# Kernel tuning notes

Hardware: AMD Instinct MI355X
Metric: run time of the kernel (lower is better)

Reference implementation:

```python
import jax, jax.numpy as jnp
import numpy as np

L, C, H, DH, LAT, N, B = 6, 768, 12, 64, 256, 65, 512


def setup_inputs() -> dict:
    key = jax.random.key(0)
    ks = jax.random.split(key, 16)
    def p(k, shape, std=0.02):
        return jax.random.normal(k, shape, jnp.float32) * std
    return {
        "x": jax.random.normal(ks[0], (B, N, C), jnp.float32),
        "ln1_g": jnp.ones((L, C), jnp.float32), "ln1_b": jnp.zeros((L, C), jnp.float32),
        "qkv_w": p(ks[1], (L, C, 3 * C)),
        "proj_w": p(ks[2], (L, C, C)),
        "qn_g": jnp.ones((L, DH), jnp.float32), "qn_b": jnp.zeros((L, DH), jnp.float32),
        "kn_g": jnp.ones((L, DH), jnp.float32), "kn_b": jnp.zeros((L, DH), jnp.float32),
        "sg_w1": p(ks[3], (L, C, 2 * LAT)),
        "sg_ln1_g": jnp.ones((L, 2 * LAT), jnp.float32), "sg_ln1_b": jnp.zeros((L, 2 * LAT), jnp.float32),
        "sg_w2": p(ks[4], (L, 2 * LAT, LAT * H)),
        "sg_ln2_g": jnp.ones((L, LAT * H), jnp.float32), "sg_ln2_b": jnp.zeros((L, LAT * H), jnp.float32),
        "sg_bias_w": p(ks[5], (L, LAT, 65 * 65), std=0.005),
        "ln2_g": jnp.ones((L, C), jnp.float32), "ln2_b": jnp.zeros((L, C), jnp.float32),
        "gate_w": p(ks[6], (L, C, 4 * C)),
        "value_w": p(ks[7], (L, C, 4 * C)),
        "out_w": p(ks[8], (L, 4 * C, C)),
    }


def _ln(x, g, b, eps=1e-5):
    # torch nn.LayerNorm: biased variance
    m = jnp.mean(x, axis=-1, keepdims=True)
    v = jnp.var(x, axis=-1, keepdims=True)
    return (x - m) * jax.lax.rsqrt(v + eps) * g + b


def _block(x, p):
    (l1g, l1b, qkvw, projw, qng, qnb, kng, knb,
     w1, s1g, s1b, w2, s2g, s2b, bw, l2g, l2b, gw, vw, ow) = p
    Bb, Nn, Cc = x.shape
    scale = DH ** -0.5
    h = _ln(x, l1g, l1b)
    cls = h[:, 0]                                     # (B, C)
    qkv = (h @ qkvw).reshape(Bb, Nn, 3, H, DH).transpose(2, 0, 3, 1, 4)
    q, k, v = qkv[0], qkv[1], qkv[2]                  # each (B, H, N, DH)
    q = _ln(q, qng, qnb) * scale
    k = _ln(k, kng, knb)
    attn = jnp.einsum('bhnd,bhmd->bhnm', q, k)        # (B, H, N, N)
    # SmolGen: CLS -> per-head additive bias
    lat1 = jax.nn.silu(_ln(cls @ w1, s1g, s1b))       # (B, 2*LAT)
    lat2 = _ln(lat1 @ w2, s2g, s2b).reshape(Bb, H, LAT)
    bias = (lat2 @ bw).reshape(Bb, H, 65, 65)
    attn = jax.nn.softmax(attn + bias[:, :, :Nn, :Nn], axis=-1)
    o = jnp.einsum('bhnm,bhmd->bhnd', attn, v)
    o = o.transpose(0, 2, 1, 3).reshape(Bb, Nn, Cc)
    x = x + o @ projw
    h2 = _ln(x, l2g, l2b)
    x = x + ((h2 @ gw) * jax.nn.silu(h2 @ vw)) @ ow   # SwiGLU
    return x, None


def reference(x, ln1_g, ln1_b, qkv_w, proj_w, qn_g, qn_b, kn_g, kn_b,
              sg_w1, sg_ln1_g, sg_ln1_b, sg_w2, sg_ln2_g, sg_ln2_b, sg_bias_w,
              ln2_g, ln2_b, gate_w, value_w, out_w):
    params = (ln1_g, ln1_b, qkv_w, proj_w, qn_g, qn_b, kn_g, kn_b,
              sg_w1, sg_ln1_g, sg_ln1_b, sg_w2, sg_ln2_g, sg_ln2_b, sg_bias_w,
              ln2_g, ln2_b, gate_w, value_w, out_w)
    out, _ = jax.lax.scan(_block, x, params)
    return out
```

## Files before the change

### kernel.cpp

```cpp
#include <hip/hip_runtime.h>
#include <hip/hip_bf16.h>


typedef __bf16 v8bf  __attribute__((ext_vector_type(8)));
typedef float  v16f  __attribute__((ext_vector_type(16)));

#define EPI_BF16      0
#define EPI_ADDF32    1
#define EPI_SILU      2
#define EPI_MUL       3
#define EPI_BF16MASK  4

__device__ __forceinline__ v16f mfma32(v8bf a, v8bf b, v16f c) {
  return __builtin_amdgcn_mfma_f32_32x32x16_bf16(a, b, c, 0, 0, 0);
}

template<int EPI>
__global__ __launch_bounds__(256, 3)
void gemm_bt(const __bf16* __restrict__ A, long long lda,
             const __bf16* __restrict__ Bt,
             void* outp, const __bf16* extra,
             int Nout, int K, int nvalid)
{
  __shared__ __align__(16) __bf16 Als[128 * 64];
  __shared__ __align__(16) __bf16 Bls[128 * 64];
  const int tid  = threadIdx.x;
  const int w    = tid >> 6, lane = tid & 63;
  const int m0   = blockIdx.y * 128, n0 = blockIdx.x * 128;
  const int wm   = (w & 1) * 64, wn = (w >> 1) * 64;
  const int l31  = lane & 31, l5 = lane >> 5;

  const __bf16* ag[4];
  const __bf16* bg[4];
#pragma unroll
  for (int i = 0; i < 4; ++i) {
    int li  = i * 256 + tid;
    int row = li >> 3;
    int c   = (li & 7) ^ (row & 7);
    ag[i] = A  + (size_t)(m0 + row) * (size_t)lda + c * 8;
    bg[i] = Bt + (size_t)(n0 + row) * (size_t)K   + c * 8;
  }
  char* alds0 = ((char*)Als) + w * 1024;
  char* blds0 = ((char*)Bls) + w * 1024;

  v16f acc[2][2] = {};

  for (int kt = 0; kt < K; kt += 64) {
#pragma unroll
    for (int i = 0; i < 4; ++i) {
      __builtin_amdgcn_global_load_lds(
          (const __attribute__((address_space(1))) void*)(ag[i]),
          (__attribute__((address_space(3))) void*)(alds0 + i * 4096), 16, 0, 0);
      __builtin_amdgcn_global_load_lds(
          (const __attribute__((address_space(1))) void*)(bg[i]),
          (__attribute__((address_space(3))) void*)(blds0 + i * 4096), 16, 0, 0);
      ag[i] += 64; bg[i] += 64;
    }
    __syncthreads();
#pragma unroll
    for (int kk = 0; kk < 4; ++kk) {
      v8bf af[2], bf[2];
#pragma unroll
      for (int t = 0; t < 2; ++t) {
        int m  = wm + t * 32 + l31;
        int ch = (kk * 2 + l5) ^ (m & 7);
        af[t] = *(const v8bf*)(Als + m * 64 + ch * 8);
        int n   = wn + t * 32 + l31;
        int ch2 = (kk * 2 + l5) ^ (n & 7);
        bf[t] = *(const v8bf*)(Bls + n * 64 + ch2 * 8);
      }
      acc[0][0] = mfma32(af[0], bf[0], acc[0][0]);
      acc[0][1] = mfma32(af[0], bf[1], acc[0][1]);
      acc[1][0] = mfma32(af[1], bf[0], acc[1][0]);
      acc[1][1] = mfma32(af[1], bf[1], acc[1][1]);
    }
    __syncthreads();
  }

#pragma unroll
  for (int mi = 0; mi < 2; ++mi)
#pragma unroll
  for (int ni = 0; ni < 2; ++ni) {
    int col  = n0 + wn + ni * 32 + l31;
    int rowb = m0 + wm + mi * 32 + 4 * l5;
#pragma unroll
    for (int r = 0; r < 16; ++r) {
      int row   = rowb + (r & 3) + 8 * (r >> 2);
      float val = acc[mi][ni][r];
      size_t idx = (size_t)row * (size_t)Nout + col;
      if (EPI == EPI_BF16) {
        ((__bf16*)outp)[idx] = (__bf16)val;
      } else if (EPI == EPI_ADDF32) {
        ((float*)outp)[idx] += val;
      } else if (EPI == EPI_SILU) {
        float s = val / (1.f + __expf(-val));
        ((__bf16*)outp)[idx] = (__bf16)s;
      } else if (EPI == EPI_MUL) {
        float e = (float)extra[idx];
        ((__bf16*)outp)[idx] = (__bf16)(val * e);
      } else {
        if (col < nvalid)
          ((__bf16*)outp)[(size_t)row * (size_t)nvalid + col] = (__bf16)val;
      }
    }
  }
}

__global__ void transpose_w(const float* __restrict__ src, __bf16* __restrict__ dst,
                            int K, int N, int Npad)
{
  __shared__ float t[32][33];
  int n0 = blockIdx.x * 32, k0 = blockIdx.y * 32;
  int tx = threadIdx.x, ty = threadIdx.y;
#pragma unroll
  for (int i = 0; i < 32; i += 8) {
    int k = k0 + ty + i, n = n0 + tx;
    t[ty + i][tx] = (k < K && n < N) ? src[(size_t)k * N + n] : 0.f;
  }
  __syncthreads();
#pragma unroll
  for (int i = 0; i < 32; i += 8) {
    int n = n0 + ty + i, k = k0 + tx;
    if (n < Npad && k < K) dst[(size_t)n * K + k] = (__bf16)t[tx][ty + i];
  }
}

__global__ __launch_bounds__(256)
void ln_f32_to_bf16(const float* __restrict__ x, const float* __restrict__ g,
                    const float* __restrict__ bb, __bf16* __restrict__ out, int C)
{
  __shared__ float sm[8];
  const float* xr = x + (size_t)blockIdx.x * C;
  float sum = 0.f, sq = 0.f;
  for (int i = threadIdx.x; i < C; i += 256) { float v = xr[i]; sum += v; sq += v * v; }
#pragma unroll
  for (int d = 1; d < 64; d <<= 1) { sum += __shfl_xor(sum, d); sq += __shfl_xor(sq, d); }
  if ((threadIdx.x & 63) == 0) { sm[threadIdx.x >> 6] = sum; sm[4 + (threadIdx.x >> 6)] = sq; }
  __syncthreads();
  sum = sm[0] + sm[1] + sm[2] + sm[3];
  sq  = sm[4] + sm[5] + sm[6] + sm[7];
  float mean = sum / C;
  float var  = sq / C - mean * mean;
  float rs   = rsqrtf(var + 1e-5f);
  __bf16* orow = out + (size_t)blockIdx.x * C;
  for (int i = threadIdx.x; i < C; i += 256)
    orow[i] = (__bf16)((xr[i] - mean) * rs * g[i] + bb[i]);
}

__global__ __launch_bounds__(256)
void ln_bf16_kernel(const __bf16* __restrict__ x, const float* __restrict__ g,
                    const float* __restrict__ bb, __bf16* __restrict__ out,
                    int C, int do_silu)
{
  __shared__ float sm[8];
  const __bf16* xr = x + (size_t)blockIdx.x * C;
  float sum = 0.f, sq = 0.f;
  for (int i = threadIdx.x; i < C; i += 256) { float v = (float)xr[i]; sum += v; sq += v * v; }
#pragma unroll
  for (int d = 1; d < 64; d <<= 1) { sum += __shfl_xor(sum, d); sq += __shfl_xor(sq, d); }
  if ((threadIdx.x & 63) == 0) { sm[threadIdx.x >> 6] = sum; sm[4 + (threadIdx.x >> 6)] = sq; }
  __syncthreads();
  sum = sm[0] + sm[1] + sm[2] + sm[3];
  sq  = sm[4] + sm[5] + sm[6] + sm[7];
  float mean = sum / C;
  float var  = sq / C - mean * mean;
  float rs   = rsqrtf(var + 1e-5f);
  __bf16* orow = out + (size_t)blockIdx.x * C;
  for (int i = threadIdx.x; i < C; i += 256) {
    float y = ((float)xr[i] - mean) * rs * g[i] + bb[i];
    if (do_silu) y = y / (1.f + __expf(-y));
    orow[i] = (__bf16)y;
  }
}

__global__ __launch_bounds__(256)
void attn_mfma(const __bf16* __restrict__ qkv,
               const float* __restrict__ qg, const float* __restrict__ qb,
               const float* __restrict__ kg, const float* __restrict__ kb,
               const __bf16* __restrict__ bias, __bf16* __restrict__ o)
{
  __shared__ __align__(16) char smem[58640];
  __bf16* qs = (__bf16*)smem;
  __bf16* ks = (__bf16*)(smem) + 96 * 64;
  __bf16* Ps = (__bf16*)smem;
  __bf16* vt = (__bf16*)(smem + 24576);
  float*  Ss = (float*)(smem + 40960);

  const int tid = threadIdx.x;
  const int bh  = blockIdx.x;
  const int b = bh / 12, h = bh % 12;
  const int w = tid >> 6, lane = tid & 63;
  const int l31 = lane & 31, l5 = lane >> 5;

  const float qgl = qg[lane], qbl = qb[lane];
  const float kgl = kg[lane], kbl = kb[lane];
  for (int n = w; n < 65; n += 4) {
    size_t src = ((size_t)(b * 65 + n)) * 2304 + h * 64 + lane;
    float qv = (float)qkv[src];
    float kv = (float)qkv[src + 768];
    float s1 = qv, s2 = qv * qv, t1 = kv, t2 = kv * kv;
#pragma unroll
    for (int d = 1; d < 64; d <<= 1) {
      s1 += __shfl_xor(s1, d); s2 += __shfl_xor(s2, d);
      t1 += __shfl_xor(t1, d); t2 += __shfl_xor(t2, d);
    }
    float qm = s1 * 0.015625f, qva = s2 * 0.015625f - qm * qm;
    float km = t1 * 0.015625f, kva = t2 * 0.015625f - km * km;
    float qrs = rsqrtf(qva + 1e-5f), krs = rsqrtf(kva + 1e-5f);
    qs[n * 64 + (((lane >> 3) ^ (n & 7)) * 8) + (lane & 7)] =
        (__bf16)(((qv - qm) * qrs * qgl + qbl) * 0.125f);
    ks[n * 64 + (((lane >> 3) ^ (n & 7)) * 8) + (lane & 7)] =
        (__bf16)((kv - km) * krs * kgl + kbl);
    vt[lane * 128 + (((n >> 3) ^ (lane & 7)) * 8) + (n & 7)] = qkv[src + 1536];
  }
  for (int e = tid; e < 64 * 31; e += 256) {
    int d = e / 31, j = 65 + e % 31;
    vt[d * 128 + (((j >> 3) ^ (d & 7)) * 8) + (j & 7)] = (__bf16)0.f;
  }
  __syncthreads();

  const __bf16* bp = bias + (size_t)bh * 4225;
  for (int t = w; t < 9; t += 4) {
    int it = t / 3, jt = t % 3;
    int mrow = it * 32 + l31;
    int nrow = jt * 32 + l31;
    v16f acc = {};
#pragma unroll
    for (int kk = 0; kk < 4; ++kk) {
      v8bf aq = *(const v8bf*)(qs + mrow * 64 + (((kk * 2 + l5) ^ (mrow & 7)) * 8));
      v8bf bk = *(const v8bf*)(ks + nrow * 64 + (((kk * 2 + l5) ^ (nrow & 7)) * 8));
      acc = mfma32(aq, bk, acc);
    }
    int j  = jt * 32 + l31;
    int ib = it * 32 + 4 * l5;
#pragma unroll
    for (int r = 0; r < 16; ++r) {
      int i = ib + (r & 3) + 8 * (r >> 2);
      if (i < 65 && j < 65)
        Ss[i * 68 + j] = acc[r] + (float)bp[i * 65 + j];
    }
  }
  __syncthreads();

  for (int i = w; i < 65; i += 4) {
    float x1 = Ss[i * 68 + lane];
    float x2 = (lane == 0) ? Ss[i * 68 + 64] : -1e30f;
    float mx = fmaxf(x1, x2);
#pragma unroll
    for (int d = 1; d < 64; d <<= 1) mx = fmaxf(mx, __shfl_xor(mx, d));
    float e1 = __expf(x1 - mx);
    float e2 = (lane == 0) ? __expf(x2 - mx) : 0.f;
    float s = e1 + e2;
#pragma unroll
    for (int d = 1; d < 64; d <<= 1) s += __shfl_xor(s, d);
    float inv = 1.f / s;
    Ps[i * 128 + (((lane >> 3) ^ (i & 7)) * 8) + (lane & 7)] = (__bf16)(e1 * inv);
    if (lane < 32) {
      int c2 = 64 + lane;
      float pv2 = (lane == 0) ? e2 * inv : 0.f;
      Ps[i * 128 + (((c2 >> 3) ^ (i & 7)) * 8) + (c2 & 7)] = (__bf16)pv2;
    }
  }
  __syncthreads();

  for (int t = w; t < 6; t += 4) {
    int it = t >> 1, dt = t & 1;
    int prow = it * 32 + l31;
    int drow = dt * 32 + l31;
    v16f acc = {};
#pragma unroll
    for (int kk = 0; kk < 6; ++kk) {
      v8bf ap = *(const v8bf*)(Ps + prow * 128 + (((kk * 2 + l5) ^ (prow & 7)) * 8));
      v8bf bv = *(const v8bf*)(vt + drow * 128 + (((kk * 2 + l5) ^ (drow & 7)) * 8));
      acc = mfma32(ap, bv, acc);
    }
    int d  = dt * 32 + l31;
    int ib = it * 32 + 4 * l5;
#pragma unroll
    for (int r = 0; r < 16; ++r) {
      int i = ib + (r & 3) + 8 * (r >> 2);
      if (i < 65)
        o[((size_t)(b * 65 + i) * 12 + h) * 64 + d] = (__bf16)acc[r];
    }
  }
}

extern "C" void kernel_launch(void* const* d_in, const int* in_sizes, int n_in,
                              void* d_out, int out_size, void* d_ws, size_t ws_size,
                              hipStream_t stream)
{
  (void)in_sizes; (void)n_in; (void)ws_size;
  const float* x_in    = (const float*)d_in[0];
  const float* ln1_g   = (const float*)d_in[1];
  const float* ln1_b   = (const float*)d_in[2];
  const float* qkv_w   = (const float*)d_in[3];
  const float* proj_w  = (const float*)d_in[4];
  const float* qn_g    = (const float*)d_in[5];
  const float* qn_b    = (const float*)d_in[6];
  const float* kn_g    = (const float*)d_in[7];
  const float* kn_b    = (const float*)d_in[8];
  const float* sg_w1   = (const float*)d_in[9];
  const float* sg_ln1g = (const float*)d_in[10];
  const float* sg_ln1b = (const float*)d_in[11];
  const float* sg_w2   = (const float*)d_in[12];
  const float* sg_ln2g = (const float*)d_in[13];
  const float* sg_ln2b = (const float*)d_in[14];
  const float* sg_bw   = (const float*)d_in[15];
  const float* ln2_g   = (const float*)d_in[16];
  const float* ln2_b   = (const float*)d_in[17];
  const float* gate_w  = (const float*)d_in[18];
  const float* value_w = (const float*)d_in[19];
  const float* out_w   = (const float*)d_in[20];

  char* ws = (char*)d_ws;
  size_t off = 0;
  auto alloc = [&](size_t bytes) -> char* {
    char* p = ws + off; off += (bytes + 255) & ~(size_t)255; return p;
  };

  __bf16* wt_qkv  = (__bf16*)alloc(2304ull * 768 * 2);
  __bf16* wt_proj = (__bf16*)alloc(768ull * 768 * 2);
  __bf16* wt_sg1  = (__bf16*)alloc(512ull * 768 * 2);
  __bf16* wt_sg2  = (__bf16*)alloc(3072ull * 512 * 2);
  __bf16* wt_bias = (__bf16*)alloc(4352ull * 256 * 2);
  __bf16* wt_gate = (__bf16*)alloc(3072ull * 768 * 2);
  __bf16* wt_val  = (__bf16*)alloc(3072ull * 768 * 2);
  __bf16* wt_out  = (__bf16*)alloc(768ull * 3072 * 2);
  __bf16* hbuf    = (__bf16*)alloc(33280ull * 768 * 2);
  __bf16* biasbuf = (__bf16*)alloc(6144ull * 4225 * 2);
  __bf16* BIG     = (__bf16*)alloc(33280ull * 2304 * 2);
  __bf16* t1buf   = (__bf16*)alloc(512ull * 512 * 2);
  __bf16* lat1    = (__bf16*)alloc(512ull * 512 * 2);
  __bf16* t2buf   = (__bf16*)alloc(512ull * 3072 * 2);
  __bf16* lat2    = (__bf16*)alloc(512ull * 3072 * 2);

  __bf16* qkvbuf = BIG;
  __bf16* mlpbuf = biasbuf;

  hipMemcpyAsync(d_out, x_in, (size_t)out_size * sizeof(float),
                 hipMemcpyDeviceToDevice, stream);
  float* xb = (float*)d_out;

  dim3 tb(32, 8);
  for (int l = 0; l < 6; ++l) {
    const float* l1g = ln1_g + l * 768;
    const float* l1b = ln1_b + l * 768;
    const float* qg  = qn_g + l * 64;
    const float* qb  = qn_b + l * 64;
    const float* kg  = kn_g + l * 64;
    const float* kb  = kn_b + l * 64;
    const float* s1g = sg_ln1g + l * 512;
    const float* s1b = sg_ln1b + l * 512;
    const float* s2g = sg_ln2g + l * 3072;
    const float* s2b = sg_ln2b + l * 3072;
    const float* l2g = ln2_g + l * 768;
    const float* l2b = ln2_b + l * 768;

    transpose_w<<<dim3(72, 24), tb, 0, stream>>>(qkv_w  + (size_t)l * 768 * 2304, wt_qkv, 768, 2304, 2304);
    transpose_w<<<dim3(24, 24), tb, 0, stream>>>(proj_w + (size_t)l * 768 * 768,  wt_proj, 768, 768, 768);
    transpose_w<<<dim3(16, 24), tb, 0, stream>>>(sg_w1  + (size_t)l * 768 * 512,  wt_sg1, 768, 512, 512);
    transpose_w<<<dim3(96, 16), tb, 0, stream>>>(sg_w2  + (size_t)l * 512 * 3072, wt_sg2, 512, 3072, 3072);
    transpose_w<<<dim3(136, 8), tb, 0, stream>>>(sg_bw  + (size_t)l * 256 * 4225, wt_bias, 256, 4225, 4352);
    transpose_w<<<dim3(96, 24), tb, 0, stream>>>(gate_w + (size_t)l * 768 * 3072, wt_gate, 768, 3072, 3072);
    transpose_w<<<dim3(96, 24), tb, 0, stream>>>(value_w+ (size_t)l * 768 * 3072, wt_val, 768, 3072, 3072);
    transpose_w<<<dim3(24, 96), tb, 0, stream>>>(out_w  + (size_t)l * 3072 * 768, wt_out, 3072, 768, 768);

    ln_f32_to_bf16<<<33280, 256, 0, stream>>>(xb, l1g, l1b, hbuf, 768);
    gemm_bt<EPI_BF16><<<dim3(18, 260), 256, 0, stream>>>(
        hbuf, 768, wt_qkv, qkvbuf, nullptr, 2304, 768, 2304);
    gemm_bt<EPI_BF16><<<dim3(4, 4), 256, 0, stream>>>(
        hbuf, 65 * 768, wt_sg1, t1buf, nullptr, 512, 768, 512);
    ln_bf16_kernel<<<512, 256, 0, stream>>>(t1buf, s1g, s1b, lat1, 512, 1);
    gemm_bt<EPI_BF16><<<dim3(24, 4), 256, 0, stream>>>(
        lat1, 512, wt_sg2, t2buf, nullptr, 3072, 512, 3072);
    ln_bf16_kernel<<<512, 256, 0, stream>>>(t2buf, s2g, s2b, lat2, 3072, 0);
    gemm_bt<EPI_BF16MASK><<<dim3(34, 48), 256, 0, stream>>>(
        lat2, 256, wt_bias, biasbuf, nullptr, 4352, 256, 4225);
    attn_mfma<<<6144, 256, 0, stream>>>(qkvbuf, qg, qb, kg, kb, biasbuf, hbuf);
    gemm_bt<EPI_ADDF32><<<dim3(6, 260), 256, 0, stream>>>(
        hbuf, 768, wt_proj, xb, nullptr, 768, 768, 768);
    ln_f32_to_bf16<<<33280, 256, 0, stream>>>(xb, l2g, l2b, hbuf, 768);
    gemm_bt<EPI_SILU><<<dim3(24, 260), 256, 0, stream>>>(
        hbuf, 768, wt_val, mlpbuf, nullptr, 3072, 768, 3072);
    gemm_bt<EPI_MUL><<<dim3(24, 260), 256, 0, stream>>>(
        hbuf, 768, wt_gate, mlpbuf, mlpbuf, 3072, 768, 3072);
    gemm_bt<EPI_ADDF32><<<dim3(6, 260), 256, 0, stream>>>(
        mlpbuf, 3072, wt_out, xb, nullptr, 768, 3072, 768);
  }
}
```

Baseline: 10.06 ms.

## Vectorize layernorm and restructure attention with register softmax and staged bias

Replaces the row-per-block f32 layernorm with a wave-per-row kernel that uses float4 loads and vector bf16 stores. The attention kernel now loads Q/K/V with 8-wide vector loads and does the per-head layernorm with an 8-lane shuffle reduction. It stages the bias tile into LDS through a padded 4232-element stride and does softmax directly on the MFMA accumulators, which drops the fp32 score buffer and one pass. The costs are a larger bias buffer, a changed V swizzle, and one warp left idle during QK^T.

```diff
diff --git a/kernel.cpp b/kernel.cpp
--- a/kernel.cpp
+++ b/kernel.cpp
@@ -3,6 +3,7 @@
 
 
 typedef __bf16 v8bf  __attribute__((ext_vector_type(8)));
+typedef __bf16 v4bf  __attribute__((ext_vector_type(4)));
 typedef float  v16f  __attribute__((ext_vector_type(16)));
 
 #define EPI_BF16      0
@@ -99,8 +100,9 @@
         float e = (float)extra[idx];
         ((__bf16*)outp)[idx] = (__bf16)(val * e);
       } else {
+        int stride = (nvalid + 7) & ~7;
         if (col < nvalid)
-          ((__bf16*)outp)[(size_t)row * (size_t)nvalid + col] = (__bf16)val;
+          ((__bf16*)outp)[(size_t)row * (size_t)stride + col] = (__bf16)val;
       }
     }
   }
@@ -126,25 +128,37 @@
 }
 
 __global__ __launch_bounds__(256)
-void ln_f32_to_bf16(const float* __restrict__ x, const float* __restrict__ g,
-                    const float* __restrict__ bb, __bf16* __restrict__ out, int C)
-{
-  __shared__ float sm[8];
-  const float* xr = x + (size_t)blockIdx.x * C;
+void ln768_f32_to_bf16(const float* __restrict__ x, const float* __restrict__ g,
+                       const float* __restrict__ bb, __bf16* __restrict__ out)
+{
+  const int row  = blockIdx.x * 4 + (threadIdx.x >> 6);
+  const int lane = threadIdx.x & 63;
+  const float* xr = x + (size_t)row * 768;
+  float4 v[3];
   float sum = 0.f, sq = 0.f;
-  for (int i = threadIdx.x; i < C; i += 256) { float v = xr[i]; sum += v; sq += v * v; }
+#pragma unroll
+  for (int c = 0; c < 3; ++c) {
+    v[c] = *(const float4*)(xr + c * 256 + lane * 4);
+    sum += v[c].x + v[c].y + v[c].z + v[c].w;
+    sq  += v[c].x * v[c].x + v[c].y * v[c].y + v[c].z * v[c].z + v[c].w * v[c].w;
+  }
 #pragma unroll
   for (int d = 1; d < 64; d <<= 1) { sum += __shfl_xor(sum, d); sq += __shfl_xor(sq, d); }
-  if ((threadIdx.x & 63) == 0) { sm[threadIdx.x >> 6] = sum; sm[4 + (threadIdx.x >> 6)] = sq; }
-  __syncthreads();
-  sum = sm[0] + sm[1] + sm[2] + sm[3];
-  sq  = sm[4] + sm[5] + sm[6] + sm[7];
-  float mean = sum / C;
-  float var  = sq / C - mean * mean;
+  float mean = sum * (1.f / 768.f);
+  float var  = sq * (1.f / 768.f) - mean * mean;
   float rs   = rsqrtf(var + 1e-5f);
-  __bf16* orow = out + (size_t)blockIdx.x * C;
-  for (int i = threadIdx.x; i < C; i += 256)
-    orow[i] = (__bf16)((xr[i] - mean) * rs * g[i] + bb[i]);
+  __bf16* orow = out + (size_t)row * 768;
+#pragma unroll
+  for (int c = 0; c < 3; ++c) {
+    float4 gv = *(const float4*)(g  + c * 256 + lane * 4);
+    float4 bv = *(const float4*)(bb + c * 256 + lane * 4);
+    v4bf o4;
+    o4[0] = (__bf16)((v[c].x - mean) * rs * gv.x + bv.x);
+    o4[1] = (__bf16)((v[c].y - mean) * rs * gv.y + bv.y);
+    o4[2] = (__bf16)((v[c].z - mean) * rs * gv.z + bv.z);
+    o4[3] = (__bf16)((v[c].w - mean) * rs * gv.w + bv.w);
+    *(v4bf*)(orow + c * 256 + lane * 4) = o4;
+  }
 }
 
 __global__ __launch_bounds__(256)
@@ -179,108 +193,145 @@
                const float* __restrict__ kg, const float* __restrict__ kb,
                const __bf16* __restrict__ bias, __bf16* __restrict__ o)
 {
-  __shared__ __align__(16) char smem[58640];
+  __shared__ __align__(16) char smem[49424];
   __bf16* qs = (__bf16*)smem;
-  __bf16* ks = (__bf16*)(smem) + 96 * 64;
+  __bf16* ks = (__bf16*)(smem + 12288);
   __bf16* Ps = (__bf16*)smem;
   __bf16* vt = (__bf16*)(smem + 24576);
-  float*  Ss = (float*)(smem + 40960);
+  __bf16* bl = (__bf16*)(smem + 40960);
 
   const int tid = threadIdx.x;
   const int bh  = blockIdx.x;
   const int b = bh / 12, h = bh % 12;
   const int w = tid >> 6, lane = tid & 63;
   const int l31 = lane & 31, l5 = lane >> 5;
-
-  const float qgl = qg[lane], qbl = qb[lane];
-  const float kgl = kg[lane], kbl = kb[lane];
-  for (int n = w; n < 65; n += 4) {
-    size_t src = ((size_t)(b * 65 + n)) * 2304 + h * 64 + lane;
-    float qv = (float)qkv[src];
-    float kv = (float)qkv[src + 768];
-    float s1 = qv, s2 = qv * qv, t1 = kv, t2 = kv * kv;
-#pragma unroll
-    for (int d = 1; d < 64; d <<= 1) {
-      s1 += __shfl_xor(s1, d); s2 += __shfl_xor(s2, d);
-      t1 += __shfl_xor(t1, d); t2 += __shfl_xor(t2, d);
-    }
-    float qm = s1 * 0.015625f, qva = s2 * 0.015625f - qm * qm;
-    float km = t1 * 0.015625f, kva = t2 * 0.015625f - km * km;
-    float qrs = rsqrtf(qva + 1e-5f), krs = rsqrtf(kva + 1e-5f);
-    qs[n * 64 + (((lane >> 3) ^ (n & 7)) * 8) + (lane & 7)] =
-        (__bf16)(((qv - qm) * qrs * qgl + qbl) * 0.125f);
-    ks[n * 64 + (((lane >> 3) ^ (n & 7)) * 8) + (lane & 7)] =
-        (__bf16)((kv - km) * krs * kgl + kbl);
-    vt[lane * 128 + (((n >> 3) ^ (lane & 7)) * 8) + (n & 7)] = qkv[src + 1536];
-  }
-  for (int e = tid; e < 64 * 31; e += 256) {
-    int d = e / 31, j = 65 + e % 31;
-    vt[d * 128 + (((j >> 3) ^ (d & 7)) * 8) + (j & 7)] = (__bf16)0.f;
+  const int li = lane & 7, rg = lane >> 3;
+
+  const __bf16* bp = bias + (size_t)bh * 4232;
+  for (int idx = tid; idx < 529; idx += 256)
+    *(v8bf*)(bl + idx * 8) = *(const v8bf*)(bp + idx * 8);
+
+  float qgv[8], qbv[8], kgv[8], kbv[8];
+#pragma unroll
+  for (int e = 0; e < 8; ++e) {
+    qgv[e] = qg[li * 8 + e]; qbv[e] = qb[li * 8 + e];
+    kgv[e] = kg[li * 8 + e]; kbv[e] = kb[li * 8 + e];
+  }
+
+  for (int n0 = 0; n0 < 65; n0 += 32) {
+    int n = n0 + w * 8 + rg;
+    if (n < 65) {
+      const __bf16* src = qkv + ((size_t)(b * 65 + n)) * 2304 + h * 64 + li * 8;
+      v8bf qv8 = *(const v8bf*)(src);
+      v8bf kv8 = *(const v8bf*)(src + 768);
+      v8bf vv8 = *(const v8bf*)(src + 1536);
+      float qf[8], kf[8];
+      float s1 = 0.f, s2 = 0.f, t1 = 0.f, t2 = 0.f;
+#pragma unroll
+      for (int e = 0; e < 8; ++e) {
+        qf[e] = (float)qv8[e]; kf[e] = (float)kv8[e];
+        s1 += qf[e]; s2 += qf[e] * qf[e];
+        t1 += kf[e]; t2 += kf[e] * kf[e];
+      }
+#pragma unroll
+      for (int d = 1; d < 8; d <<= 1) {
+        s1 += __shfl_xor(s1, d); s2 += __shfl_xor(s2, d);
+        t1 += __shfl_xor(t1, d); t2 += __shfl_xor(t2, d);
+      }
+      float qm = s1 * 0.015625f, qva = s2 * 0.015625f - qm * qm;
+      float km = t1 * 0.015625f, kva = t2 * 0.015625f - km * km;
+      float qrs = rsqrtf(qva + 1e-5f), krs = rsqrtf(kva + 1e-5f);
+      v8bf qo, ko;
+#pragma unroll
+      for (int e = 0; e < 8; ++e) {
+        qo[e] = (__bf16)(((qf[e] - qm) * qrs * qgv[e] + qbv[e]) * 0.125f);
+        ko[e] = (__bf16)((kf[e] - km) * krs * kgv[e] + kbv[e]);
+      }
+      *(v8bf*)(qs + n * 64 + (li ^ (n & 7)) * 8) = qo;
+      *(v8bf*)(ks + n * 64 + (li ^ (n & 7)) * 8) = ko;
+#pragma unroll
+      for (int e = 0; e < 8; ++e) {
+        int d = li * 8 + e;
+        int swz = (d & 7) ^ (d >> 3);
+        vt[d * 128 + (((n >> 3) ^ swz) * 8) + (n & 7)] = vv8[e];
+      }
+    }
+  }
+  for (int e2 = tid; e2 < 64 * 31; e2 += 256) {
+    int d = e2 / 31, j = 65 + e2 % 31;
+    int swz = (d & 7) ^ (d >> 3);
+    vt[d * 128 + (((j >> 3) ^ swz) * 8) + (j & 7)] = (__bf16)0.f;
   }
   __syncthreads();
 
-  const __bf16* bp = bias + (size_t)bh * 4225;
-  for (int t = w; t < 9; t += 4) {
-    int it = t / 3, jt = t % 3;
-    int mrow = it * 32 + l31;
-    int nrow = jt * 32 + l31;
-    v16f acc = {};
+  v16f s0 = {}, s1v = {}, s2v = {};
+  if (w < 3) {
+    const int mrow = w * 32 + l31;
 #pragma unroll
     for (int kk = 0; kk < 4; ++kk) {
-      v8bf aq = *(const v8bf*)(qs + mrow * 64 + (((kk * 2 + l5) ^ (mrow & 7)) * 8));
-      v8bf bk = *(const v8bf*)(ks + nrow * 64 + (((kk * 2 + l5) ^ (nrow & 7)) * 8));
-      acc = mfma32(aq, bk, acc);
-    }
-    int j  = jt * 32 + l31;
-    int ib = it * 32 + 4 * l5;
+      int lc = kk * 2 + l5;
+      v8bf aq = *(const v8bf*)(qs + mrow * 64 + ((lc ^ (mrow & 7)) * 8));
+      v8bf b0 = *(const v8bf*)(ks + (l31) * 64      + ((lc ^ ((l31) & 7)) * 8));
+      v8bf b1 = *(const v8bf*)(ks + (32 + l31) * 64 + ((lc ^ ((32 + l31) & 7)) * 8));
+      v8bf b2 = *(const v8bf*)(ks + (64 + l31) * 64 + ((lc ^ ((64 + l31) & 7)) * 8));
+      s0  = mfma32(aq, b0, s0);
+      s1v = mfma32(aq, b1, s1v);
+      s2v = mfma32(aq, b2, s2v);
+    }
+  }
+  __syncthreads();
+
+  if (w < 3) {
+    const int j0 = l31, j1 = 32 + l31, j2 = 64 + l31;
 #pragma unroll
     for (int r = 0; r < 16; ++r) {
-      int i = ib + (r & 3) + 8 * (r >> 2);
-      if (i < 65 && j < 65)
-        Ss[i * 68 + j] = acc[r] + (float)bp[i * 65 + j];
+      int i = w * 32 + 4 * l5 + (r & 3) + 8 * (r >> 2);
+      float v0 = s0[r], v1 = s1v[r], v2 = s2v[r];
+      if (i < 65) {
+        v0 += (float)bl[i * 65 + j0];
+        v1 += (float)bl[i * 65 + j1];
+        if (l31 == 0) v2 += (float)bl[i * 65 + 64];
+      }
+      float vx = (l31 == 0) ? v2 : -1e30f;
+      float mx = fmaxf(fmaxf(v0, v1), vx);
+#pragma unroll
+      for (int d = 1; d < 32; d <<= 1) mx = fmaxf(mx, __shfl_xor(mx, d));
+      float e0 = __expf(v0 - mx);
+      float e1 = __expf(v1 - mx);
+      float e2 = (l31 == 0) ? __expf(v2 - mx) : 0.f;
+      float sum = e0 + e1 + e2;
+#pragma unroll
+      for (int d = 1; d < 32; d <<= 1) sum += __shfl_xor(sum, d);
+      float inv = 1.f / sum;
+      Ps[i * 128 + (((j0 >> 3) ^ (i & 7)) * 8) + (j0 & 7)] = (__bf16)(e0 * inv);
+      Ps[i * 128 + (((j1 >> 3) ^ (i & 7)) * 8) + (j1 & 7)] = (__bf16)(e1 * inv);
+      Ps[i * 128 + (((j2 >> 3) ^ (i & 7)) * 8) + (j2 & 7)] =
+          (__bf16)((l31 == 0) ? e2 * inv : 0.f);
     }
   }
   __syncthreads();
 
-  for (int i = w; i < 65; i += 4) {
-    float x1 = Ss[i * 68 + lane];
-    float x2 = (lane == 0) ? Ss[i * 68 + 64] : -1e30f;
-    float mx = fmaxf(x1, x2);
-#pragma unroll
-    for (int d = 1; d < 64; d <<= 1) mx = fmaxf(mx, __shfl_xor(mx, d));
-    float e1 = __expf(x1 - mx);
-    float e2 = (lane == 0) ? __expf(x2 - mx) : 0.f;
-    float s = e1 + e2;
-#pragma unroll
-    for (int d = 1; d < 64; d <<= 1) s += __shfl_xor(s, d);
-    float inv = 1.f / s;
-    Ps[i * 128 + (((lane >> 3) ^ (i & 7)) * 8) + (lane & 7)] = (__bf16)(e1 * inv);
-    if (lane < 32) {
-      int c2 = 64 + lane;
-      float pv2 = (lane == 0) ? e2 * inv : 0.f;
-      Ps[i * 128 + (((c2 >> 3) ^ (i & 7)) * 8) + (c2 & 7)] = (__bf16)pv2;
-    }
-  }
-  __syncthreads();
-
-  for (int t = w; t < 6; t += 4) {
+  const int nt = (w < 2) ? 2 : 1;
+  for (int tt = 0; tt < nt; ++tt) {
+    int t = w + tt * 4;
     int it = t >> 1, dt = t & 1;
     int prow = it * 32 + l31;
     int drow = dt * 32 + l31;
+    int dswz = (drow & 7) ^ (drow >> 3);
     v16f acc = {};
 #pragma unroll
     for (int kk = 0; kk < 6; ++kk) {
-      v8bf ap = *(const v8bf*)(Ps + prow * 128 + (((kk * 2 + l5) ^ (prow & 7)) * 8));
-      v8bf bv = *(const v8bf*)(vt + drow * 128 + (((kk * 2 + l5) ^ (drow & 7)) * 8));
+      int lc = kk * 2 + l5;
+      v8bf ap = *(const v8bf*)(Ps + prow * 128 + ((lc ^ (prow & 7)) * 8));
+      v8bf bv = *(const v8bf*)(vt + drow * 128 + ((lc ^ dswz) * 8));
       acc = mfma32(ap, bv, acc);
     }
-    int d  = dt * 32 + l31;
-    int ib = it * 32 + 4 * l5;
+    int dcol = dt * 32 + l31;
 #pragma unroll
     for (int r = 0; r < 16; ++r) {
-      int i = ib + (r & 3) + 8 * (r >> 2);
+      int i = it * 32 + 4 * l5 + (r & 3) + 8 * (r >> 2);
       if (i < 65)
-        o[((size_t)(b * 65 + i) * 12 + h) * 64 + d] = (__bf16)acc[r];
+        o[((size_t)(b * 65 + i) * 12 + h) * 64 + dcol] = (__bf16)acc[r];
     }
   }
 }
@@ -327,7 +378,7 @@
   __bf16* wt_val  = (__bf16*)alloc(3072ull * 768 * 2);
   __bf16* wt_out  = (__bf16*)alloc(768ull * 3072 * 2);
   __bf16* hbuf    = (__bf16*)alloc(33280ull * 768 * 2);
-  __bf16* biasbuf = (__bf16*)alloc(6144ull * 4225 * 2);
+  __bf16* biasbuf = (__bf16*)alloc(6144ull * 4232 * 2);
   __bf16* BIG     = (__bf16*)alloc(33280ull * 2304 * 2);
   __bf16* t1buf   = (__bf16*)alloc(512ull * 512 * 2);
   __bf16* lat1    = (__bf16*)alloc(512ull * 512 * 2);
@@ -365,7 +416,7 @@
     transpose_w<<<dim3(96, 24), tb, 0, stream>>>(value_w+ (size_t)l * 768 * 3072, wt_val, 768, 3072, 3072);
     transpose_w<<<dim3(24, 96), tb, 0, stream>>>(out_w  + (size_t)l * 3072 * 768, wt_out, 3072, 768, 768);
 
-    ln_f32_to_bf16<<<33280, 256, 0, stream>>>(xb, l1g, l1b, hbuf, 768);
+    ln768_f32_to_bf16<<<8320, 256, 0, stream>>>(xb, l1g, l1b, hbuf);
     gemm_bt<EPI_BF16><<<dim3(18, 260), 256, 0, stream>>>(
         hbuf, 768, wt_qkv, qkvbuf, nullptr, 2304, 768, 2304);
     gemm_bt<EPI_BF16><<<dim3(4, 4), 256, 0, stream>>>(
@@ -379,7 +430,7 @@
     attn_mfma<<<6144, 256, 0, stream>>>(qkvbuf, qg, qb, kg, kb, biasbuf, hbuf);
     gemm_bt<EPI_ADDF32><<<dim3(6, 260), 256, 0, stream>>>(
         hbuf, 768, wt_proj, xb, nullptr, 768, 768, 768);
-    ln_f32_to_bf16<<<33280, 256, 0, stream>>>(xb, l2g, l2b, hbuf, 768);
+    ln768_f32_to_bf16<<<8320, 256, 0, stream>>>(xb, l2g, l2b, hbuf);
     gemm_bt<EPI_SILU><<<dim3(24, 260), 256, 0, stream>>>(
         hbuf, 768, wt_val, mlpbuf, nullptr, 3072, 768, 3072);
     gemm_bt<EPI_MUL><<<dim3(24, 260), 256, 0, stream>>>(
```

New measurement: 8.208 ms. 18.4% less time.
